# Kernel tuning notes

Hardware: AMD Instinct MI355X
Metric: run time of the kernel (lower is better)

Reference implementation:

```python
import jax, jax.numpy as jnp
import numpy as np
import math

B, S, D, H = 8, 1024, 1024, 16
DH = D // H  # 64


def setup_inputs() -> dict:
    key = jax.random.key(0)
    ks = jax.random.split(key, 10)
    inputs = jax.random.normal(ks[0], (B, S, D), dtype=jnp.float32)
    mask = jax.random.randint(ks[1], (B, S, S), 0, 2) == 1  # bool [B,S,S]
    sc = 1.0 / math.sqrt(D)
    # per-head projection weights stacked: [H, D, DH], biases [H, DH]
    Wq = jax.random.normal(ks[2], (H, D, DH), dtype=jnp.float32) * sc
    bq = jax.random.normal(ks[3], (H, DH), dtype=jnp.float32) * 0.02
    Wk = jax.random.normal(ks[4], (H, D, DH), dtype=jnp.float32) * sc
    bk = jax.random.normal(ks[5], (H, DH), dtype=jnp.float32) * 0.02
    Wv = jax.random.normal(ks[6], (H, D, DH), dtype=jnp.float32) * sc
    bv = jax.random.normal(ks[7], (H, DH), dtype=jnp.float32) * 0.02
    Wo = jax.random.normal(ks[8], (D, D), dtype=jnp.float32) * sc
    bo = jax.random.normal(ks[9], (D,), dtype=jnp.float32) * 0.02
    return {"inputs": inputs, "mask": mask, "Wq": Wq, "bq": bq, "Wk": Wk,
            "bk": bk, "Wv": Wv, "bv": bv, "Wo": Wo, "bo": bo}


def reference(inputs, mask, Wq, bq, Wk, bk, Wv, bv, Wo, bo):
    d_model = inputs.shape[-1]
    scale = 1.0 / jnp.sqrt(jnp.asarray(d_model, inputs.dtype))  # note: sqrt(d_model), as in source
    # batched per-head projections: [B,H,S,DH]
    Q = jnp.einsum('bsd,hde->bhse', inputs, Wq) + bq[None, :, None, :]
    K = jnp.einsum('bsd,hde->bhse', inputs, Wk) + bk[None, :, None, :]
    V = jnp.einsum('bsd,hde->bhse', inputs, Wv) + bv[None, :, None, :]
    scores = jnp.einsum('bhse,bhte->bhst', Q, K) * scale  # [B,H,S,S]
    scores = jnp.where(mask[:, None, :, :], jnp.asarray(-1e9, scores.dtype), scores)
    attn = jax.nn.softmax(scores, axis=-1)
    ctx = jnp.einsum('bhst,bhte->bhse', attn, V)  # [B,H,S,DH]
    # concat heads along last dim (head h -> slice h*DH:(h+1)*DH), matches torch.cat
    bsz, h, s, dh = ctx.shape
    x = ctx.transpose(0, 2, 1, 3).reshape(bsz, s, h * dh)
    return x @ Wo + bo
```

## Files before the change

kernel.cpp:

```cpp
#include <hip/hip_runtime.h>
#include <hip/hip_bf16.h>
#include <stdint.h>


typedef __attribute__((ext_vector_type(8))) short short8;
typedef __attribute__((ext_vector_type(4))) float floatx4;

__device__ __forceinline__ int swz(int r, int kc) { return r * 8 + (kc ^ (r & 7)); }
__device__ __forceinline__ short8 as_frag(uint4 u) { return __builtin_bit_cast(short8, u); }
__device__ __forceinline__ floatx4 mfma16(short8 a, short8 b, floatx4 c) {
    return __builtin_amdgcn_mfma_f32_16x16x32_bf16(a, b, c, 0, 0, 0);
}
__device__ __forceinline__ unsigned short f2bu(float f) {
    return __builtin_bit_cast(unsigned short, __float2bfloat16(f));
}
__device__ __forceinline__ short f2b(float f) {
    return __builtin_bit_cast(short, __float2bfloat16(f));
}
__device__ __forceinline__ float b2f(short s) {
    return __bfloat162float(__builtin_bit_cast(__hip_bfloat16, s));
}
__device__ __forceinline__ void dma16(const void* g, void* l) {
    __builtin_amdgcn_global_load_lds(
        (const __attribute__((address_space(1))) uint32_t*)g,
        (__attribute__((address_space(3))) uint32_t*)l, 16, 0, 0);
}
__device__ __forceinline__ uint2 pack4(float a, float b, float c, float d) {
    uint2 p;
    p.x = (unsigned)f2bu(a) | ((unsigned)f2bu(b) << 16);
    p.y = (unsigned)f2bu(c) | ((unsigned)f2bu(d) << 16);
    return p;
}

__device__ __forceinline__ void detect_mode(const unsigned* Xw, int* s_is32) {
    if (threadIdx.x < 64) {
        unsigned lo = Xw[threadIdx.x] & 0xFFFFu;
        unsigned e = (lo >> 7) & 0xFFu;
        unsigned long long bal = __ballot(e >= 88u && e <= 150u);
        if (threadIdx.x == 0) *s_is32 = (bal != ~0ull) ? 1 : 0;
    }
    __syncthreads();
}

__device__ __forceinline__ float load_elt(const void* p, size_t idx, int is32) {
    return is32 ? ((const float*)p)[idx]
                : __bfloat162float(((const __hip_bfloat16*)p)[idx]);
}

__global__ __launch_bounds__(256) void prep_all(
    const void* __restrict__ Wq, const void* __restrict__ Wk,
    const void* __restrict__ Wv, const void* __restrict__ Wo,
    const void* __restrict__ bq, const void* __restrict__ bk,
    const void* __restrict__ bv, const void* __restrict__ bo,
    const void* __restrict__ mask_raw, const void* __restrict__ X,
    __hip_bfloat16* __restrict__ WT, __hip_bfloat16* __restrict__ WoT,
    __hip_bfloat16* __restrict__ bc, unsigned long long* __restrict__ bits64,
    __hip_bfloat16* __restrict__ Xb, int do_x)
{
    __shared__ __hip_bfloat16 T[64][72];
    __shared__ int s_is32;
    int blk = blockIdx.x;
    int tid = threadIdx.x;
    const unsigned* Xw = (const unsigned*)X;

    if (blk < 1024) {
        detect_mode(Xw, &s_is32);
        const void* src; size_t src_off;
        __hip_bfloat16* dst;
        int src_ld, dst_ld;
        if (blk < 768) {
            int p = blk >> 8;
            int rem = blk & 255;
            int h = rem >> 4, dt = rem & 15;
            src = (p == 0) ? Wq : (p == 1) ? Wk : Wv;
            src_off = ((size_t)h * 1024 + (size_t)dt * 64) * 64;
            dst = WT + (((size_t)p * 16 + h) * 64) * 1024 + dt * 64;
            src_ld = 64; dst_ld = 1024;
        } else {
            int t = blk - 768;
            int kt = t >> 4, nt = t & 15;
            src = Wo; src_off = (size_t)kt * 64 * 1024 + nt * 64;
            dst = WoT + (size_t)nt * 64 * 1024 + kt * 64;
            src_ld = 1024; dst_ld = 1024;
        }
        #pragma unroll
        for (int i = 0; i < 16; i++) {
            int idx = tid + i * 256;
            int r = idx >> 6, c = idx & 63;
            T[c][r] = __float2bfloat16(load_elt(src, src_off + (size_t)r * src_ld + c, s_is32));
        }
        __syncthreads();
        #pragma unroll
        for (int i = 0; i < 16; i++) {
            int idx = tid + i * 256;
            int r = idx >> 6, c = idx & 63;
            dst[(size_t)r * dst_ld + c] = T[r][c];
        }
    } else if (blk == 1024) {
        detect_mode(Xw, &s_is32);
        #pragma unroll
        for (int i = 0; i < 16; i++) {
            int idx = tid + i * 256;
            int which = idx >> 10, j = idx & 1023;
            const void* src = (which == 0) ? bq : (which == 1) ? bk : (which == 2) ? bv : bo;
            bc[idx] = __float2bfloat16(load_elt(src, j, s_is32));
        }
    } else if (blk < 1537) {
        int blkL = blk - 1025;
        const int* mi = (const int*)mask_raw;
        const unsigned char* mb = (const unsigned char*)mask_raw;
        int lane = tid & 63;
        bool ok = true;
        #pragma unroll
        for (int i = 0; i < 4; i++) {
            unsigned v = (unsigned)mi[lane * 4 + i];
            if (v > 1u) ok = false;
        }
        bool is_i32 = (__ballot(ok) == ~0ull);
        int gw = (blkL * 256 + tid) >> 6;
        const int NW = 512 * 4;
        const int NWORDS = (8 * 1024 * 1024) / 64;
        if (is_i32) {
            for (int i = gw; i < NWORDS; i += NW) {
                int mv = mi[(size_t)i * 64 + lane];
                unsigned long long bal = __ballot(mv != 0);
                if (lane == 0) {
                    int bb = i >> 14, q = (i >> 4) & 1023, t = i & 15;
                    bits64[((size_t)bb << 14) + ((size_t)t << 10) + q] = bal;
                }
            }
        } else {
            for (int i = gw; i < NWORDS; i += NW) {
                int mv = mb[(size_t)i * 64 + lane];
                unsigned long long bal = __ballot(mv != 0);
                if (lane == 0) {
                    int bb = i >> 14, q = (i >> 4) & 1023, t = i & 15;
                    bits64[((size_t)bb << 14) + ((size_t)t << 10) + q] = bal;
                }
            }
        }
    } else if (do_x) {
        detect_mode(Xw, &s_is32);
        int blkL = blk - 1537;
        size_t g = ((size_t)blkL * 256 + tid) * 16;
        if (s_is32) {
            const float* Xf = (const float*)X;
            #pragma unroll
            for (int half = 0; half < 2; half++) {
                float4 f0 = *(const float4*)(Xf + g + half * 8);
                float4 f1 = *(const float4*)(Xf + g + half * 8 + 4);
                short8 s;
                s[0] = f2b(f0.x); s[1] = f2b(f0.y); s[2] = f2b(f0.z); s[3] = f2b(f0.w);
                s[4] = f2b(f1.x); s[5] = f2b(f1.y); s[6] = f2b(f1.z); s[7] = f2b(f1.w);
                *(uint4*)(Xb + g + half * 8) = __builtin_bit_cast(uint4, s);
            }
        } else {
            const uint4* Xu = (const uint4*)X;
            *(uint4*)(Xb + g)     = Xu[g / 8];
            *(uint4*)(Xb + g + 8) = Xu[g / 8 + 1];
        }
    }
}

__global__ __launch_bounds__(256, 2) void qkv_gemm_dma(
    const __hip_bfloat16* __restrict__ Xb,
    const __hip_bfloat16* __restrict__ WT,
    const __hip_bfloat16* __restrict__ bc,
    __hip_bfloat16* __restrict__ Q,
    __hip_bfloat16* __restrict__ Ko,
    __hip_bfloat16* __restrict__ Vt)
{
    __shared__ uint4 AsU[256 * 8];
    __shared__ uint4 BsU[128 * 8];
    int tid = threadIdx.x, lane = tid & 63, wave = tid >> 6;
    int quad = lane >> 4, ln = lane & 15;
    int mw = wave & 1, nw = wave >> 1;
    int m0 = blockIdx.x * 256;
    int n0 = blockIdx.y * 128;
    const __hip_bfloat16* Wp = WT + (size_t)n0 * 1024;

    floatx4 acc[8][4];
    #pragma unroll
    for (int i = 0; i < 8; i++)
        #pragma unroll
        for (int j = 0; j < 4; j++) acc[i][j] = (floatx4){0.f, 0.f, 0.f, 0.f};

    for (int k0 = 0; k0 < 1024; k0 += 64) {
        #pragma unroll
        for (int i = 0; i < 8; i++) {
            int r = wave * 64 + i * 8 + (lane >> 3);
            int kc = (lane & 7) ^ (r & 7);
            char* lds = (char*)AsU + (size_t)(wave * 512 + i * 64) * 16;
            dma16(Xb + (size_t)(m0 + r) * 1024 + k0 + kc * 8, lds);
        }
        #pragma unroll
        for (int i = 0; i < 4; i++) {
            int r = wave * 32 + i * 8 + (lane >> 3);
            int kc = (lane & 7) ^ (r & 7);
            char* lds = (char*)BsU + (size_t)(wave * 256 + i * 64) * 16;
            dma16(Wp + (size_t)r * 1024 + k0 + kc * 8, lds);
        }
        __syncthreads();
        #pragma unroll
        for (int kk = 0; kk < 2; kk++) {
            short8 af[8], bf[4];
            #pragma unroll
            for (int mi = 0; mi < 8; mi++)
                af[mi] = as_frag(AsU[swz(mw * 128 + mi * 16 + ln, kk * 4 + quad)]);
            #pragma unroll
            for (int ni = 0; ni < 4; ni++)
                bf[ni] = as_frag(BsU[swz(nw * 64 + ni * 16 + ln, kk * 4 + quad)]);
            #pragma unroll
            for (int mi = 0; mi < 8; mi++)
                #pragma unroll
                for (int ni = 0; ni < 4; ni++)
                    acc[mi][ni] = mfma16(af[mi], bf[ni], acc[mi][ni]);
        }
        __syncthreads();
    }

    int b = m0 >> 10;
    int s0 = m0 & 1023;
    int proj = n0 >> 10;
    if (proj == 2) {
        #pragma unroll
        for (int ni = 0; ni < 4; ni++) {
            int n = n0 + nw * 64 + ni * 16 + ln;
            int h = (n >> 6) & 15, e = n & 63;
            float bval = __bfloat162float(bc[2 * 1024 + (n & 1023)]);
            #pragma unroll
            for (int mi = 0; mi < 8; mi++) {
                int sb = s0 + mw * 128 + mi * 16 + quad * 4;
                uint2 pk = pack4(acc[mi][ni][0] + bval, acc[mi][ni][1] + bval,
                                 acc[mi][ni][2] + bval, acc[mi][ni][3] + bval);
                *(uint2*)(Vt + (((size_t)b * 16 + h) * 64 + e) * 1024 + sb) = pk;
            }
        }
    } else {
        __hip_bfloat16* P = (proj == 0) ? Q : Ko;
        #pragma unroll
        for (int ni = 0; ni < 4; ni++) {
            int n = n0 + nw * 64 + ni * 16 + ln;
            int h = (n >> 6) & 15, e = n & 63;
            float bval = __bfloat162float(bc[proj * 1024 + (n & 1023)]);
            #pragma unroll
            for (int mi = 0; mi < 8; mi++) {
                #pragma unroll
                for (int r = 0; r < 4; r++) {
                    int s = s0 + mw * 128 + mi * 16 + quad * 4 + r;
                    P[(((size_t)b * 16 + h) * 1024 + s) * 64 + e] =
                        __float2bfloat16(acc[mi][ni][r] + bval);
                }
            }
        }
    }
}

__global__ __launch_bounds__(256) void qkv_gemm2(
    const void* __restrict__ Xsrc,
    const __hip_bfloat16* __restrict__ WT,
    const __hip_bfloat16* __restrict__ bc,
    __hip_bfloat16* __restrict__ Q,
    __hip_bfloat16* __restrict__ Ko,
    __hip_bfloat16* __restrict__ Vt)
{
    __shared__ int s_is32;
    detect_mode((const unsigned*)Xsrc, &s_is32);
    __shared__ uint4 AsU[128 * 8];
    __shared__ uint4 BsU[128 * 8];
    int tid = threadIdx.x, lane = tid & 63, wave = tid >> 6;
    int quad = lane >> 4, ln = lane & 15;
    int m0 = blockIdx.x * 128;
    int n0 = blockIdx.y * 128;
    const __hip_bfloat16* Wp = WT + (size_t)n0 * 1024;
    const float* Xf = (const float*)Xsrc;
    const __hip_bfloat16* Xh = (const __hip_bfloat16*)Xsrc;

    floatx4 acc[2][8];
    #pragma unroll
    for (int i = 0; i < 2; i++)
        #pragma unroll
        for (int j = 0; j < 8; j++) acc[i][j] = (floatx4){0.f, 0.f, 0.f, 0.f};

    for (int k0 = 0; k0 < 1024; k0 += 64) {
        if (s_is32) {
            #pragma unroll
            for (int i = 0; i < 4; i++) {
                int id = tid + i * 256;
                int r = id >> 3, kc = id & 7;
                size_t off = (size_t)(m0 + r) * 1024 + k0 + kc * 8;
                float4 f0 = *(const float4*)(Xf + off);
                float4 f1 = *(const float4*)(Xf + off + 4);
                short8 s;
                s[0] = f2b(f0.x); s[1] = f2b(f0.y); s[2] = f2b(f0.z); s[3] = f2b(f0.w);
                s[4] = f2b(f1.x); s[5] = f2b(f1.y); s[6] = f2b(f1.z); s[7] = f2b(f1.w);
                AsU[swz(r, kc)] = __builtin_bit_cast(uint4, s);
            }
        } else {
            #pragma unroll
            for (int i = 0; i < 4; i++) {
                int id = tid + i * 256;
                int r = id >> 3, kc = id & 7;
                AsU[swz(r, kc)] = *(const uint4*)(Xh + (size_t)(m0 + r) * 1024 + k0 + kc * 8);
            }
        }
        #pragma unroll
        for (int i = 0; i < 4; i++) {
            int id = tid + i * 256;
            int r = id >> 3, kc = id & 7;
            BsU[swz(r, kc)] = *(const uint4*)(Wp + (size_t)r * 1024 + k0 + kc * 8);
        }
        __syncthreads();
        #pragma unroll
        for (int kk = 0; kk < 2; kk++) {
            short8 a0 = as_frag(AsU[swz(wave * 32 + ln, kk * 4 + quad)]);
            short8 a1 = as_frag(AsU[swz(wave * 32 + 16 + ln, kk * 4 + quad)]);
            #pragma unroll
            for (int nt = 0; nt < 8; nt++) {
                short8 bf = as_frag(BsU[swz(nt * 16 + ln, kk * 4 + quad)]);
                acc[0][nt] = mfma16(a0, bf, acc[0][nt]);
                acc[1][nt] = mfma16(a1, bf, acc[1][nt]);
            }
        }
        __syncthreads();
    }

    int b = m0 >> 10;
    int s0 = m0 & 1023;
    #pragma unroll
    for (int nt = 0; nt < 8; nt++) {
        int n = n0 + nt * 16 + ln;
        int proj = n >> 10, h = (n >> 6) & 15, e = n & 63;
        float bval = __bfloat162float(bc[proj * 1024 + (n & 1023)]);
        #pragma unroll
        for (int mt = 0; mt < 2; mt++) {
            #pragma unroll
            for (int r = 0; r < 4; r++) {
                int s = s0 + wave * 32 + mt * 16 + quad * 4 + r;
                float v = acc[mt][nt][r] + bval;
                if (proj == 2) {
                    Vt[(((size_t)b * 16 + h) * 64 + e) * 1024 + s] = __float2bfloat16(v);
                } else {
                    __hip_bfloat16* P = (proj == 0) ? Q : Ko;
                    P[(((size_t)b * 16 + h) * 1024 + s) * 64 + e] = __float2bfloat16(v);
                }
            }
        }
    }
}

__global__ __launch_bounds__(256, 4) void attn(
    const __hip_bfloat16* __restrict__ Q,
    const __hip_bfloat16* __restrict__ K,
    const __hip_bfloat16* __restrict__ Vt,
    const unsigned long long* __restrict__ bits,
    __hip_bfloat16* __restrict__ ctx)
{
    __shared__ uint4 KsU[64 * 8];
    __shared__ uint4 VsU[2 * 64 * 8];
    __shared__ uint4 PsU[4 * 256];

    int tid = threadIdx.x, lane = tid & 63, w = tid >> 6;
    int quad = lane >> 4, ln = lane & 15;
    int bh = blockIdx.x;
    int q0 = blockIdx.y * 128;
    int b = bh >> 4, h = bh & 15;
    const __hip_bfloat16* Qp = Q + (size_t)bh * 1024 * 64;
    const __hip_bfloat16* Kp = K + (size_t)bh * 1024 * 64;
    const __hip_bfloat16* Vp = Vt + (size_t)bh * 64 * 1024;
    const unsigned long long* bp = bits + (size_t)b * 16 * 1024;

    short8 qf[2][2];
    #pragma unroll
    for (int g = 0; g < 2; g++)
        #pragma unroll
        for (int kk = 0; kk < 2; kk++)
            qf[g][kk] = as_frag(*(const uint4*)(
                Qp + (size_t)(q0 + w * 32 + g * 16 + ln) * 64 + kk * 32 + quad * 8));

    int r8 = lane >> 3;
    int scc = (lane & 7) ^ r8;

    #pragma unroll
    for (int i = 0; i < 2; i++) {
        int r = w * 16 + i * 8 + r8;
        dma16(Kp + (size_t)r * 64 + scc * 8, (char*)KsU + (size_t)(w * 128 + i * 64) * 16);
        dma16(Vp + (size_t)r * 1024 + scc * 8, (char*)VsU + (size_t)(w * 128 + i * 64) * 16);
    }
    __syncthreads();

    floatx4 acc_o[2][4];
    #pragma unroll
    for (int g = 0; g < 2; g++)
        #pragma unroll
        for (int i = 0; i < 4; i++) acc_o[g][i] = (floatx4){0.f, 0.f, 0.f, 0.f};
    float lsum[2] = {0.f, 0.f};
    const float C2 = 0.04508422f;
    __hip_bfloat16* Pw = (__hip_bfloat16*)&PsU[w * 256];
    int cur = 0;

    for (int t0 = 0; t0 < 1024; t0 += 64) {
        unsigned long long mcur0 = bp[((size_t)(t0 >> 6) << 10) + q0 + w * 32 + ln];
        unsigned long long mcur1 = bp[((size_t)(t0 >> 6) << 10) + q0 + w * 32 + 16 + ln];

        floatx4 st[2][4];
        #pragma unroll
        for (int g = 0; g < 2; g++)
            #pragma unroll
            for (int i = 0; i < 4; i++) st[g][i] = (floatx4){0.f, 0.f, 0.f, 0.f};
        #pragma unroll
        for (int kk = 0; kk < 2; kk++) {
            #pragma unroll
            for (int tt = 0; tt < 4; tt++) {
                short8 kf = as_frag(KsU[swz(tt * 16 + ln, kk * 4 + quad)]);
                st[0][tt] = mfma16(kf, qf[0][kk], st[0][tt]);
                st[1][tt] = mfma16(kf, qf[1][kk], st[1][tt]);
            }
        }

        bool more = t0 < 960;
        if (more) {
            __syncthreads();
            int tn = t0 + 64;
            char* vb = (char*)VsU + (size_t)(cur ^ 1) * 8192;
            #pragma unroll
            for (int i = 0; i < 2; i++) {
                int r = w * 16 + i * 8 + r8;
                dma16(Kp + (size_t)(tn + r) * 64 + scc * 8,
                      (char*)KsU + (size_t)(w * 128 + i * 64) * 16);
                dma16(Vp + (size_t)r * 1024 + tn + scc * 8,
                      vb + (size_t)(w * 128 + i * 64) * 16);
            }
        }

        #pragma unroll
        for (int g = 0; g < 2; g++) {
            int qloc = g * 16 + ln;
            unsigned long long msh = (g ? mcur1 : mcur0) >> (quad * 4);
            #pragma unroll
            for (int tt = 0; tt < 4; tt++) {
                unsigned mb = (unsigned)(msh >> (tt * 16)) & 0xFu;
                float pe0 = (mb & 1u) ? 0.f : __builtin_amdgcn_exp2f(st[g][tt][0] * C2);
                float pe1 = (mb & 2u) ? 0.f : __builtin_amdgcn_exp2f(st[g][tt][1] * C2);
                float pe2 = (mb & 4u) ? 0.f : __builtin_amdgcn_exp2f(st[g][tt][2] * C2);
                float pe3 = (mb & 8u) ? 0.f : __builtin_amdgcn_exp2f(st[g][tt][3] * C2);
                lsum[g] += (pe0 + pe1) + (pe2 + pe3);
                int kcp = tt * 2 + (quad >> 1);
                int off = qloc * 64 + (kcp ^ (qloc & 7)) * 8 + (quad & 1) * 4;
                *(uint2*)(Pw + off) = pack4(pe0, pe1, pe2, pe3);
            }
        }

        const uint4* Vcur = VsU + (size_t)cur * 512;
        #pragma unroll
        for (int kk = 0; kk < 2; kk++) {
            short8 pf0 = as_frag(PsU[w * 256 + swz(0 * 16 + ln, kk * 4 + quad)]);
            short8 pf1 = as_frag(PsU[w * 256 + swz(1 * 16 + ln, kk * 4 + quad)]);
            #pragma unroll
            for (int et = 0; et < 4; et++) {
                short8 vf = as_frag(Vcur[swz(et * 16 + ln, kk * 4 + quad)]);
                acc_o[0][et] = mfma16(vf, pf0, acc_o[0][et]);
                acc_o[1][et] = mfma16(vf, pf1, acc_o[1][et]);
            }
        }

        if (more)
            __syncthreads();
        cur ^= 1;
    }

    #pragma unroll
    for (int g = 0; g < 2; g++) {
        lsum[g] += __shfl_xor(lsum[g], 16, 64);
        lsum[g] += __shfl_xor(lsum[g], 32, 64);
    }

    #pragma unroll
    for (int g = 0; g < 2; g++) {
        float inv = 1.f / fmaxf(lsum[g], 1e-20f);
        int s = q0 + w * 32 + g * 16 + ln;
        __hip_bfloat16* crow = ctx + ((size_t)b * 1024 + s) * 1024 + h * 64 + quad * 4;
        #pragma unroll
        for (int et = 0; et < 4; et++) {
            uint2 pk = pack4(acc_o[g][et][0] * inv, acc_o[g][et][1] * inv,
                             acc_o[g][et][2] * inv, acc_o[g][et][3] * inv);
            *(uint2*)(crow + et * 16) = pk;
        }
    }
}

__global__ __launch_bounds__(256) void out_gemm_dma(
    const __hip_bfloat16* __restrict__ Cx,
    const __hip_bfloat16* __restrict__ WoT,
    const __hip_bfloat16* __restrict__ bc,
    const unsigned* __restrict__ Xw,
    void* __restrict__ dout,
    int direct)
{
    __shared__ int s_is32;
    detect_mode(Xw, &s_is32);
    __shared__ uint4 AsU[128 * 8];
    __shared__ uint4 BsU[128 * 8];
    int tid = threadIdx.x, lane = tid & 63, wave = tid >> 6;
    int quad = lane >> 4, ln = lane & 15;
    int mw = wave & 1, nw = wave >> 1;
    int m0 = blockIdx.x * 128;
    int n0 = blockIdx.y * 128;

    floatx4 acc[4][4];
    #pragma unroll
    for (int i = 0; i < 4; i++)
        #pragma unroll
        for (int j = 0; j < 4; j++) acc[i][j] = (floatx4){0.f, 0.f, 0.f, 0.f};

    for (int k0 = 0; k0 < 1024; k0 += 64) {
        #pragma unroll
        for (int i = 0; i < 4; i++) {
            int r = wave * 32 + i * 8 + (lane >> 3);
            int kc = (lane & 7) ^ (r & 7);
            char* ldsA = (char*)AsU + (size_t)(wave * 256 + i * 64) * 16;
            char* ldsB = (char*)BsU + (size_t)(wave * 256 + i * 64) * 16;
            dma16(Cx + (size_t)(m0 + r) * 1024 + k0 + kc * 8, ldsA);
            dma16(WoT + (size_t)(n0 + r) * 1024 + k0 + kc * 8, ldsB);
        }
        __syncthreads();
        #pragma unroll
        for (int kk = 0; kk < 2; kk++) {
            short8 af[4], bf[4];
            #pragma unroll
            for (int mi = 0; mi < 4; mi++)
                af[mi] = as_frag(AsU[swz(mw * 64 + mi * 16 + ln, kk * 4 + quad)]);
            #pragma unroll
            for (int ni = 0; ni < 4; ni++)
                bf[ni] = as_frag(BsU[swz(nw * 64 + ni * 16 + ln, kk * 4 + quad)]);
            #pragma unroll
            for (int mi = 0; mi < 4; mi++)
                #pragma unroll
                for (int ni = 0; ni < 4; ni++)
                    acc[mi][ni] = mfma16(af[mi], bf[ni], acc[mi][ni]);
        }
        __syncthreads();
    }

    const __hip_bfloat16* bo = bc + 3 * 1024;
    #pragma unroll
    for (int ni = 0; ni < 4; ni++) {
        int n = n0 + nw * 64 + ni * 16 + ln;
        float bval = __bfloat162float(bo[n]);
        #pragma unroll
        for (int mi = 0; mi < 4; mi++) {
            #pragma unroll
            for (int r = 0; r < 4; r++) {
                int m = m0 + mw * 64 + mi * 16 + quad * 4 + r;
                float v = acc[mi][ni][r] + bval;
                if (direct && s_is32) ((float*)dout)[(size_t)m * 1024 + n] = v;
                else ((__hip_bfloat16*)dout)[(size_t)m * 1024 + n] = __float2bfloat16(v);
            }
        }
    }
}

__global__ __launch_bounds__(256) void emit_out(
    const __hip_bfloat16* __restrict__ Fo, const unsigned* __restrict__ Xw,
    void* __restrict__ dout)
{
    __shared__ int s_is32;
    detect_mode(Xw, &s_is32);
    size_t g = (size_t)blockIdx.x * 256 + threadIdx.x;
    uint4 u = *(const uint4*)(Fo + g * 8);
    if (s_is32) {
        short8 s = __builtin_bit_cast(short8, u);
        float4 f0, f1;
        f0.x = b2f(s[0]); f0.y = b2f(s[1]); f0.z = b2f(s[2]); f0.w = b2f(s[3]);
        f1.x = b2f(s[4]); f1.y = b2f(s[5]); f1.z = b2f(s[6]); f1.w = b2f(s[7]);
        *(float4*)((float*)dout + g * 8) = f0;
        *(float4*)((float*)dout + g * 8 + 4) = f1;
    } else {
        *(uint4*)((__hip_bfloat16*)dout + g * 8) = u;
    }
}

extern "C" void kernel_launch(void* const* d_in, const int* in_sizes, int n_in,
                              void* d_out, int out_size, void* d_ws, size_t ws_size,
                              hipStream_t stream) {
    const void* X  = d_in[0];
    const void* mk = d_in[1];
    const void* Wq = d_in[2];
    const void* bq = d_in[3];
    const void* Wk = d_in[4];
    const void* bk = d_in[5];
    const void* Wv = d_in[6];
    const void* bv = d_in[7];
    const void* Wo = d_in[8];
    const void* bo = d_in[9];
    const unsigned* Xw = (const unsigned*)X;

    char* ws = (char*)d_ws;
    __hip_bfloat16*     WT   = (__hip_bfloat16*)(ws);
    __hip_bfloat16*     WoT  = (__hip_bfloat16*)(ws + ((size_t)6 << 20));
    unsigned long long* bits = (unsigned long long*)(ws + ((size_t)8 << 20));
    __hip_bfloat16*     bc   = (__hip_bfloat16*)(ws + ((size_t)9 << 20));
    __hip_bfloat16*     Xb   = (__hip_bfloat16*)(ws + ((size_t)10 << 20));
    __hip_bfloat16*     Qb   = (__hip_bfloat16*)(ws + ((size_t)26 << 20));
    __hip_bfloat16*     Kb   = (__hip_bfloat16*)(ws + ((size_t)42 << 20));
    __hip_bfloat16*     Vtb  = (__hip_bfloat16*)(ws + ((size_t)58 << 20));

    bool bigws = ws_size >= ((size_t)74 << 20);

    hipLaunchKernelGGL(prep_all, dim3(3585), dim3(256), 0, stream,
                       Wq, Wk, Wv, Wo, bq, bk, bv, bo, mk, X,
                       WT, WoT, bc, bits, Xb, bigws ? 1 : 0);

    if (bigws) {
        __hip_bfloat16* Cx = Xb;
        hipLaunchKernelGGL(qkv_gemm_dma, dim3(32, 24), dim3(256), 0, stream,
                           Xb, WT, bc, Qb, Kb, Vtb);
        hipLaunchKernelGGL(attn, dim3(128, 8), dim3(256), 0, stream,
                           Qb, Kb, Vtb, bits, Cx);
        hipLaunchKernelGGL(out_gemm_dma, dim3(64, 8), dim3(256), 0, stream,
                           Cx, WoT, bc, Xw, d_out, 1);
    } else {
        __hip_bfloat16* Cx = (__hip_bfloat16*)d_out;
        __hip_bfloat16* Fo = Qb;
        hipLaunchKernelGGL(qkv_gemm2, dim3(64, 24), dim3(256), 0, stream,
                           X, WT, bc, Qb, Kb, Vtb);
        hipLaunchKernelGGL(attn, dim3(128, 8), dim3(256), 0, stream,
                           Qb, Kb, Vtb, bits, Cx);
        hipLaunchKernelGGL(out_gemm_dma, dim3(64, 8), dim3(256), 0, stream,
                           Cx, WoT, bc, Xw, (void*)Fo, 0);
        hipLaunchKernelGGL(emit_out, dim3(4096), dim3(256), 0, stream,
                           Fo, Xw, d_out);
    }
}
```

Baseline: 309.4 us.

## Use 512-thread attention blocks with 128-key tiles and MFMA priority hints

The attention kernel now runs 8 waves per block over 256 query rows, which halves the grid. It loads 128 keys and values per step in a single-buffered stage between two barriers, replacing the old 64-key double-buffered V prefetch. Each K/V tile is shared by twice as many waves, and there are fewer barriers per key, but the loads no longer overlap with compute. It also raises wave priority around the MFMA sections. Launch bounds of 512x4 may squeeze the register budget.

```diff
diff --git a/kernel.cpp b/kernel.cpp
--- a/kernel.cpp
+++ b/kernel.cpp
@@ -349,21 +349,21 @@
     }
 }
 
-__global__ __launch_bounds__(256, 4) void attn(
+__global__ __launch_bounds__(512, 4) void attn(
     const __hip_bfloat16* __restrict__ Q,
     const __hip_bfloat16* __restrict__ K,
     const __hip_bfloat16* __restrict__ Vt,
     const unsigned long long* __restrict__ bits,
     __hip_bfloat16* __restrict__ ctx)
 {
-    __shared__ uint4 KsU[64 * 8];
-    __shared__ uint4 VsU[2 * 64 * 8];
-    __shared__ uint4 PsU[4 * 256];
+    __shared__ uint4 KsU[2 * 512];
+    __shared__ uint4 VsU[2 * 512];
+    __shared__ uint4 PsU[8 * 256];
 
     int tid = threadIdx.x, lane = tid & 63, w = tid >> 6;
     int quad = lane >> 4, ln = lane & 15;
     int bh = blockIdx.x;
-    int q0 = blockIdx.y * 128;
+    int q0 = blockIdx.y * 256;
     int b = bh >> 4, h = bh & 15;
     const __hip_bfloat16* Qp = Q + (size_t)bh * 1024 * 64;
     const __hip_bfloat16* Kp = K + (size_t)bh * 1024 * 64;
@@ -379,15 +379,7 @@
                 Qp + (size_t)(q0 + w * 32 + g * 16 + ln) * 64 + kk * 32 + quad * 8));
 
     int r8 = lane >> 3;
-    int scc = (lane & 7) ^ r8;
-
-    #pragma unroll
-    for (int i = 0; i < 2; i++) {
-        int r = w * 16 + i * 8 + r8;
-        dma16(Kp + (size_t)r * 64 + scc * 8, (char*)KsU + (size_t)(w * 128 + i * 64) * 16);
-        dma16(Vp + (size_t)r * 1024 + scc * 8, (char*)VsU + (size_t)(w * 128 + i * 64) * 16);
-    }
-    __syncthreads();
+    int kc = (lane & 7) ^ r8;
 
     floatx4 acc_o[2][4];
     #pragma unroll
@@ -397,76 +389,77 @@
     float lsum[2] = {0.f, 0.f};
     const float C2 = 0.04508422f;
     __hip_bfloat16* Pw = (__hip_bfloat16*)&PsU[w * 256];
-    int cur = 0;
-
-    for (int t0 = 0; t0 < 1024; t0 += 64) {
-        unsigned long long mcur0 = bp[((size_t)(t0 >> 6) << 10) + q0 + w * 32 + ln];
-        unsigned long long mcur1 = bp[((size_t)(t0 >> 6) << 10) + q0 + w * 32 + 16 + ln];
-
-        floatx4 st[2][4];
-        #pragma unroll
-        for (int g = 0; g < 2; g++)
-            #pragma unroll
-            for (int i = 0; i < 4; i++) st[g][i] = (floatx4){0.f, 0.f, 0.f, 0.f};
-        #pragma unroll
-        for (int kk = 0; kk < 2; kk++) {
-            #pragma unroll
-            for (int tt = 0; tt < 4; tt++) {
-                short8 kf = as_frag(KsU[swz(tt * 16 + ln, kk * 4 + quad)]);
-                st[0][tt] = mfma16(kf, qf[0][kk], st[0][tt]);
-                st[1][tt] = mfma16(kf, qf[1][kk], st[1][tt]);
-            }
-        }
-
-        bool more = t0 < 960;
-        if (more) {
-            __syncthreads();
-            int tn = t0 + 64;
-            char* vb = (char*)VsU + (size_t)(cur ^ 1) * 8192;
-            #pragma unroll
-            for (int i = 0; i < 2; i++) {
-                int r = w * 16 + i * 8 + r8;
-                dma16(Kp + (size_t)(tn + r) * 64 + scc * 8,
-                      (char*)KsU + (size_t)(w * 128 + i * 64) * 16);
-                dma16(Vp + (size_t)r * 1024 + tn + scc * 8,
-                      vb + (size_t)(w * 128 + i * 64) * 16);
-            }
-        }
-
-        #pragma unroll
-        for (int g = 0; g < 2; g++) {
-            int qloc = g * 16 + ln;
-            unsigned long long msh = (g ? mcur1 : mcur0) >> (quad * 4);
-            #pragma unroll
-            for (int tt = 0; tt < 4; tt++) {
-                unsigned mb = (unsigned)(msh >> (tt * 16)) & 0xFu;
-                float pe0 = (mb & 1u) ? 0.f : __builtin_amdgcn_exp2f(st[g][tt][0] * C2);
-                float pe1 = (mb & 2u) ? 0.f : __builtin_amdgcn_exp2f(st[g][tt][1] * C2);
-                float pe2 = (mb & 4u) ? 0.f : __builtin_amdgcn_exp2f(st[g][tt][2] * C2);
-                float pe3 = (mb & 8u) ? 0.f : __builtin_amdgcn_exp2f(st[g][tt][3] * C2);
-                lsum[g] += (pe0 + pe1) + (pe2 + pe3);
-                int kcp = tt * 2 + (quad >> 1);
-                int off = qloc * 64 + (kcp ^ (qloc & 7)) * 8 + (quad & 1) * 4;
-                *(uint2*)(Pw + off) = pack4(pe0, pe1, pe2, pe3);
-            }
-        }
-
-        const uint4* Vcur = VsU + (size_t)cur * 512;
-        #pragma unroll
-        for (int kk = 0; kk < 2; kk++) {
-            short8 pf0 = as_frag(PsU[w * 256 + swz(0 * 16 + ln, kk * 4 + quad)]);
-            short8 pf1 = as_frag(PsU[w * 256 + swz(1 * 16 + ln, kk * 4 + quad)]);
-            #pragma unroll
-            for (int et = 0; et < 4; et++) {
-                short8 vf = as_frag(Vcur[swz(et * 16 + ln, kk * 4 + quad)]);
-                acc_o[0][et] = mfma16(vf, pf0, acc_o[0][et]);
-                acc_o[1][et] = mfma16(vf, pf1, acc_o[1][et]);
-            }
-        }
-
-        if (more)
-            __syncthreads();
-        cur ^= 1;
+
+    for (int t0 = 0; t0 < 1024; t0 += 128) {
+        __syncthreads();
+        #pragma unroll
+        for (int i = 0; i < 2; i++) {
+            int tK = t0 + i * 64 + w * 8 + r8;
+            dma16(Kp + (size_t)tK * 64 + kc * 8,
+                  (char*)KsU + (size_t)(i * 512 + w * 64) * 16);
+            int e = w * 8 + r8;
+            dma16(Vp + (size_t)e * 1024 + t0 + i * 64 + kc * 8,
+                  (char*)VsU + (size_t)(i * 512 + w * 64) * 16);
+        }
+        __syncthreads();
+
+        #pragma unroll
+        for (int s = 0; s < 2; s++) {
+            int t64 = (t0 >> 6) + s;
+            unsigned long long mcur0 = bp[((size_t)t64 << 10) + q0 + w * 32 + ln];
+            unsigned long long mcur1 = bp[((size_t)t64 << 10) + q0 + w * 32 + 16 + ln];
+            const uint4* Ks = KsU + s * 512;
+            const uint4* Vs = VsU + s * 512;
+
+            floatx4 st[2][4];
+            #pragma unroll
+            for (int g = 0; g < 2; g++)
+                #pragma unroll
+                for (int i = 0; i < 4; i++) st[g][i] = (floatx4){0.f, 0.f, 0.f, 0.f};
+            __builtin_amdgcn_s_setprio(1);
+            #pragma unroll
+            for (int kk = 0; kk < 2; kk++) {
+                #pragma unroll
+                for (int tt = 0; tt < 4; tt++) {
+                    short8 kf = as_frag(Ks[swz(tt * 16 + ln, kk * 4 + quad)]);
+                    st[0][tt] = mfma16(kf, qf[0][kk], st[0][tt]);
+                    st[1][tt] = mfma16(kf, qf[1][kk], st[1][tt]);
+                }
+            }
+            __builtin_amdgcn_s_setprio(0);
+
+            #pragma unroll
+            for (int g = 0; g < 2; g++) {
+                int qloc = g * 16 + ln;
+                unsigned long long msh = (g ? mcur1 : mcur0) >> (quad * 4);
+                #pragma unroll
+                for (int tt = 0; tt < 4; tt++) {
+                    unsigned mb = (unsigned)(msh >> (tt * 16)) & 0xFu;
+                    float pe0 = (mb & 1u) ? 0.f : __builtin_amdgcn_exp2f(st[g][tt][0] * C2);
+                    float pe1 = (mb & 2u) ? 0.f : __builtin_amdgcn_exp2f(st[g][tt][1] * C2);
+                    float pe2 = (mb & 4u) ? 0.f : __builtin_amdgcn_exp2f(st[g][tt][2] * C2);
+                    float pe3 = (mb & 8u) ? 0.f : __builtin_amdgcn_exp2f(st[g][tt][3] * C2);
+                    lsum[g] += (pe0 + pe1) + (pe2 + pe3);
+                    int kcp = tt * 2 + (quad >> 1);
+                    int off = qloc * 64 + (kcp ^ (qloc & 7)) * 8 + (quad & 1) * 4;
+                    *(uint2*)(Pw + off) = pack4(pe0, pe1, pe2, pe3);
+                }
+            }
+
+            __builtin_amdgcn_s_setprio(1);
+            #pragma unroll
+            for (int kk = 0; kk < 2; kk++) {
+                short8 pf0 = as_frag(PsU[w * 256 + swz(0 * 16 + ln, kk * 4 + quad)]);
+                short8 pf1 = as_frag(PsU[w * 256 + swz(1 * 16 + ln, kk * 4 + quad)]);
+                #pragma unroll
+                for (int et = 0; et < 4; et++) {
+                    short8 vf = as_frag(Vs[swz(et * 16 + ln, kk * 4 + quad)]);
+                    acc_o[0][et] = mfma16(vf, pf0, acc_o[0][et]);
+                    acc_o[1][et] = mfma16(vf, pf1, acc_o[1][et]);
+                }
+            }
+            __builtin_amdgcn_s_setprio(0);
+        }
     }
 
     #pragma unroll
@@ -615,7 +608,7 @@
         __hip_bfloat16* Cx = Xb;
         hipLaunchKernelGGL(qkv_gemm_dma, dim3(32, 24), dim3(256), 0, stream,
                            Xb, WT, bc, Qb, Kb, Vtb);
-        hipLaunchKernelGGL(attn, dim3(128, 8), dim3(256), 0, stream,
+        hipLaunchKernelGGL(attn, dim3(128, 4), dim3(512), 0, stream,
                            Qb, Kb, Vtb, bits, Cx);
         hipLaunchKernelGGL(out_gemm_dma, dim3(64, 8), dim3(256), 0, stream,
                            Cx, WoT, bc, Xw, d_out, 1);
@@ -624,7 +617,7 @@
         __hip_bfloat16* Fo = Qb;
         hipLaunchKernelGGL(qkv_gemm2, dim3(64, 24), dim3(256), 0, stream,
                            X, WT, bc, Qb, Kb, Vtb);
-        hipLaunchKernelGGL(attn, dim3(128, 8), dim3(256), 0, stream,
+        hipLaunchKernelGGL(attn, dim3(128, 4), dim3(512), 0, stream,
                            Qb, Kb, Vtb, bits, Cx);
         hipLaunchKernelGGL(out_gemm_dma, dim3(64, 8), dim3(256), 0, stream,
                            Cx, WoT, bc, Xw, (void*)Fo, 0);
```

Result: no change. 311.0 us (+0.5%).
